# Performance work log

Measured on AMD Instinct MI355X. Metric: run time of the kernel, lower is better.

Reference implementation:

```python
import jax, jax.numpy as jnp
import numpy as np

B, S, H, T = 64, 512, 768, 50


def setup_inputs() -> dict:
    key = jax.random.key(0)
    k1, k2, k3, k4, k5, k6, k7 = jax.random.split(key, 7)
    full_hidden = jax.random.normal(k1, (B, S, H), dtype=jnp.float32)
    tag_ids = jax.random.randint(k2, (B, S), 0, T)
    lengths = jax.random.randint(k3, (B,), 1, S + 1)
    mask = (jnp.arange(S)[None, :] < lengths[:, None])  # valid-prefix mask, t=0 always on
    W = jax.random.normal(k4, (H, T), dtype=jnp.float32) * 0.02
    b = jnp.zeros((T,), dtype=jnp.float32)
    start_transitions = jax.random.normal(k5, (T,), dtype=jnp.float32) * 0.1
    end_transitions = jax.random.normal(k6, (T,), dtype=jnp.float32) * 0.1
    transitions = jax.random.normal(k7, (T, T), dtype=jnp.float32) * 0.1
    return {
        'full_hidden': full_hidden, 'W': W, 'b': b,
        'start_transitions': start_transitions, 'end_transitions': end_transitions,
        'transitions': transitions, 'tag_ids': tag_ids, 'mask': mask,
    }


def _crf_losses(emissions, start_transitions, end_transitions, transitions, tag_ids, mask):
    # emissions: [B,S,T]; returns per-sequence loss = log_partition - gold_score (pytorch-crf, reduction='none', negated)
    maskf = mask.astype(emissions.dtype)
    Bn = tag_ids.shape[0]
    bidx = jnp.arange(Bn)
    # ---- numerator: score of the gold tag path ----
    em_tag = jnp.take_along_axis(emissions, tag_ids[..., None], axis=2)[..., 0]  # [B,S]
    num = start_transitions[tag_ids[:, 0]] + em_tag[:, 0]
    trans_score = transitions[tag_ids[:, :-1], tag_ids[:, 1:]]  # [B,S-1]
    num = num + jnp.sum((trans_score + em_tag[:, 1:]) * maskf[:, 1:], axis=1)
    lengths = jnp.sum(mask.astype(jnp.int32), axis=1)
    last_tags = tag_ids[bidx, lengths - 1]
    num = num + end_transitions[last_tags]
    # ---- denominator: log partition via forward DP (scan over time) ----
    alpha0 = start_transitions[None, :] + emissions[:, 0]  # [B,T]

    def step(alpha, inp):
        em_t, m_t = inp  # [B,T], [B]
        nxt = jax.nn.logsumexp(alpha[:, :, None] + transitions[None, :, :] + em_t[:, None, :], axis=1)
        alpha = jnp.where(m_t[:, None], nxt, alpha)
        return alpha, None

    em_rest = jnp.swapaxes(emissions[:, 1:], 0, 1)  # [S-1,B,T]
    m_rest = jnp.swapaxes(mask[:, 1:], 0, 1)        # [S-1,B]
    alpha, _ = jax.lax.scan(step, alpha0, (em_rest, m_rest))
    den = jax.nn.logsumexp(alpha + end_transitions[None, :], axis=1)
    return den - num  # [B]


def reference(full_hidden, W, b, start_transitions, end_transitions, transitions, tag_ids, mask):
    # dropout is identity in eval mode (config dropout applied at train time only)
    emissions = jnp.einsum('bsh,ht->bst', full_hidden, W) + b  # hid2tag
    return _crf_losses(emissions, start_transitions, end_transitions, transitions, tag_ids, mask)
```

## Files before the change

### kernel.cpp

```cpp
#include <hip/hip_runtime.h>
#include <cstdint>
#include <cstddef>

#define Bn 64
#define Sn 512
#define Hn 768
#define Tn 50
#define CH 32
#define NCH 16

typedef short short8 __attribute__((ext_vector_type(8)));
typedef float floatx4 __attribute__((ext_vector_type(4)));

__device__ __forceinline__ uint32_t rne_bf16(float x) {
  uint32_t u = __float_as_uint(x);
  return (u + 0x7FFFu + ((u >> 16) & 1u)) >> 16;
}
__device__ __forceinline__ uint32_t pack2(float a, float b) {
  return rne_bf16(a) | (rne_bf16(b) << 16);
}
__device__ __forceinline__ float rdlane(float v, int i) {
  return __uint_as_float(__builtin_amdgcn_readlane(__float_as_uint(v), i));
}

__global__ __launch_bounds__(256) void prep_kernel(
    const float* __restrict__ W, const int* __restrict__ mask,
    uint32_t* __restrict__ wfrag, int* __restrict__ lenbuf) {
  const int blk = blockIdx.x;
  const int tid = threadIdx.x;
  if (blk < 64) {
    if (tid < 64) {
      int s = 0;
      for (int t = tid; t < Sn; t += 64) s += mask[blk * Sn + t];
#pragma unroll
      for (int off = 1; off < 64; off <<= 1) s += __shfl_xor(s, off);
      if (tid == 0) lenbuf[blk] = s;
    }
    return;
  }
  const int gid = (blk - 64) * 256 + tid;
  const int f = gid >> 6;
  const int l = gid & 63;
  const int ks = f >> 2, nt = f & 3;
  const int col = nt * 16 + (l & 15);
  const int k0 = ks * 32 + (l >> 4) * 8;
  float v[8];
#pragma unroll
  for (int j = 0; j < 8; ++j)
    v[j] = (col < Tn) ? W[(size_t)(k0 + j) * Tn + col] : 0.f;
  uint4 d;
  d.x = pack2(v[0], v[1]);
  d.y = pack2(v[2], v[3]);
  d.z = pack2(v[4], v[5]);
  d.w = pack2(v[6], v[7]);
  ((uint4*)wfrag)[gid] = d;
}

#define BK 64
__global__ __launch_bounds__(256) void emissions_kernel(
    const float* __restrict__ hidden, const uint32_t* __restrict__ wfrag,
    const float* __restrict__ bias, const int* __restrict__ lenbuf,
    float* __restrict__ em) {
  const int blk = blockIdx.x;
  const int bb = blk >> 3, c = blk & 7;
  if (c * 64 >= lenbuf[bb]) return;
  const int tid = threadIdx.x;
  const int lane = tid & 63;
  const int w = tid >> 6;
  const int g = lane >> 4;
  const int li = lane & 15;
  const int row0 = blk * 64;
  __shared__ char lds_raw[64 * 128];

  floatx4 acc[4];
#pragma unroll
  for (int nt = 0; nt < 4; ++nt) acc[nt] = (floatx4)0.f;

  const float* hbase = hidden + (size_t)row0 * Hn;
  const short8* wf = (const short8*)wfrag;

  float4 pf[4];
#pragma unroll
  for (int k = 0; k < 4; ++k)
    pf[k] = *(const float4*)(hbase + (size_t)(w * 16 + 4 * k + g) * Hn + li * 4);

  for (int ch = 0; ch < Hn / BK; ++ch) {
#pragma unroll
    for (int k = 0; k < 4; ++k) {
      const int r = w * 16 + 4 * k + g;
      const uint32_t b0 = pack2(pf[k].x, pf[k].y);
      const uint32_t b1 = pack2(pf[k].z, pf[k].w);
      const int byteoff = r * 128 + ((li * 8) ^ ((r & 7) << 4));
      *(uint2*)(lds_raw + byteoff) = make_uint2(b0, b1);
    }
    if (ch + 1 < Hn / BK) {
      const int kc = (ch + 1) * BK;
#pragma unroll
      for (int k = 0; k < 4; ++k)
        pf[k] = *(const float4*)(hbase + (size_t)(w * 16 + 4 * k + g) * Hn + kc +
                                 li * 4);
    }
    asm volatile("s_waitcnt lgkmcnt(0)" ::: "memory");
#pragma unroll
    for (int ks = 0; ks < 2; ++ks) {
      const int r = w * 16 + li;
      const int kb = ks * 64 + g * 16;
      const short8 af =
          *(const short8*)(lds_raw + r * 128 + (kb ^ ((r & 7) << 4)));
      const int ksg = ch * 2 + ks;
#pragma unroll
      for (int nt = 0; nt < 4; ++nt) {
        const short8 bf = wf[(ksg * 4 + nt) * 64 + lane];
        acc[nt] =
            __builtin_amdgcn_mfma_f32_16x16x32_bf16(af, bf, acc[nt], 0, 0, 0);
      }
    }
  }
#pragma unroll
  for (int nt = 0; nt < 4; ++nt) {
    const int col = nt * 16 + li;
    if (col < Tn) {
      const float bs = bias[col];
#pragma unroll
      for (int r = 0; r < 4; ++r) {
        const int row = row0 + w * 16 + g * 4 + r;
        em[(size_t)row * Tn + col] = acc[nt][r] + bs;
      }
    }
  }
}

__global__ __launch_bounds__(64) void scan_kernel(
    const float* __restrict__ em, const float* __restrict__ startT,
    const float* __restrict__ trans, const int* __restrict__ tag,
    const int* __restrict__ lenbuf, float* __restrict__ fvec,
    float* __restrict__ gvec, float* __restrict__ Lf,
    float* __restrict__ numpart) {
  const int blk = blockIdx.x;
  const int b = blk >> 5;
  const int c = (blk >> 1) & (NCH - 1);
  const int dir = blk & 1;
  const int len = lenbuf[b];
  const int t0 = 1 + c * CH;
  if (t0 >= len) return;
  if (dir && c == 0) return;
  const int t1 = (t0 + CH < len) ? t0 + CH : len;
  const int L = t1 - t0;
  const int lane = threadIdx.x;
  const int jc = lane < Tn ? lane : 0;
  const bool live = lane < Tn;
  const float* emb = em + (size_t)b * Sn * Tn;

  if (!dir) {
    float npv = 0.f;
    if (lane < L) {
      const int t = t0 + lane;
      const int tp = tag[b * Sn + t - 1], tc = tag[b * Sn + t];
      npv = trans[tp * Tn + tc] + emb[(size_t)t * Tn + tc];
    }
#pragma unroll
    for (int off = 1; off < 64; off <<= 1) npv += __shfl_xor(npv, off);
    if (lane == 0) numpart[b * NCH + c] = npv;
  }

  float e[Tn];
#pragma unroll
  for (int i = 0; i < Tn; ++i) {
    e[i] = __expf(dir ? trans[jc * Tn + i] : trans[i * Tn + jc]);
    asm volatile("" : "+v"(e[i]));
  }

  float Cacc = 0.f;
  float q;
  if (!dir)
    q = live ? (c == 0 ? __expf(startT[jc] + emb[jc]) : 1.f) : 0.f;
  else
    q = live ? 1.f : 0.f;

#define T_OF(k) (dir ? (t1 - 1 - (k)) : (t0 + (k)))
  float ld1 = emb[(size_t)T_OF(0) * Tn + jc];
  const float ld2 = emb[(size_t)T_OF(L > 1 ? 1 : 0) * Tn + jc];
  float ee = live ? __expf(ld1) : 0.f;
  ld1 = ld2;

  for (int k = 0; k < L; ++k) {
    const float ee_cur = ee;
    const int kn = (k + 2 < L) ? k + 2 : L - 1;
    const float ldn = emb[(size_t)T_OF(kn) * Tn + jc];
    ee = live ? __expf(ld1) : 0.f;
    ld1 = ldn;

    const float x = dir ? ee_cur * q : q;
    float s0 = 0.f, s1 = 0.f, s2 = 0.f, s3 = 0.f;
#pragma unroll
    for (int i = 0; i < 48; i += 4) {
      s0 = fmaf(rdlane(x, i + 0), e[i + 0], s0);
      s1 = fmaf(rdlane(x, i + 1), e[i + 1], s1);
      s2 = fmaf(rdlane(x, i + 2), e[i + 2], s2);
      s3 = fmaf(rdlane(x, i + 3), e[i + 3], s3);
    }
    s0 = fmaf(rdlane(x, 48), e[48], s0);
    s1 = fmaf(rdlane(x, 49), e[49], s1);
    const float s = (s0 + s1) + (s2 + s3);
    q = dir ? s : ee_cur * s;

    if ((k & 7) == 7) {
      float M = q;
#pragma unroll
      for (int off = 1; off < 64; off <<= 1) M = fmaxf(M, __shfl_xor(M, off));
      const float r = __builtin_amdgcn_rcpf(M);
      q *= r;
      Cacc -= __logf(r);
    }
  }
#undef T_OF

  float M = q;
#pragma unroll
  for (int off = 1; off < 64; off <<= 1) M = fmaxf(M, __shfl_xor(M, off));
  const float r = __builtin_amdgcn_rcpf(M);
  const float qn = live ? q * r : 0.f;
  Cacc -= __logf(r);
  if (dir) {
    gvec[((size_t)b * NCH + c) * 64 + lane] = qn;
  } else {
    fvec[((size_t)b * NCH + c) * 64 + lane] = qn;
    if (lane == 0) Lf[b * NCH + c] = Cacc;
  }
}

__global__ __launch_bounds__(64) void stitch_kernel(
    const float* __restrict__ em, const float* __restrict__ startT,
    const float* __restrict__ endT, const float* __restrict__ trans,
    const int* __restrict__ tag, const int* __restrict__ lenbuf,
    const float* __restrict__ fvec, const float* __restrict__ gvec,
    const float* __restrict__ Lf, const float* __restrict__ numpart,
    float* __restrict__ out) {
  const int b = blockIdx.x;
  const int lane = threadIdx.x;
  const int len = lenbuf[b];
  const int C = (len - 1 + CH - 1) / CH;
  const int jc = lane < Tn ? lane : 0;
  const bool live = lane < Tn;
  const float* emb = em + (size_t)b * Sn * Tn;

  float np = (lane < C) ? numpart[b * NCH + lane] : 0.f;
#pragma unroll
  for (int off = 1; off < 64; off <<= 1) np += __shfl_xor(np, off);
  const int tg0 = tag[b * Sn];
  const int tgl = tag[b * Sn + len - 1];
  np += startT[tg0] + emb[tg0] + endT[tgl];

  float den;
  if (C == 0) {
    float v = live ? (startT[jc] + emb[jc] + endT[jc]) : -INFINITY;
    float M = v;
#pragma unroll
    for (int off = 1; off < 64; off <<= 1) M = fmaxf(M, __shfl_xor(M, off));
    float s = __expf(v - M);
#pragma unroll
    for (int off = 1; off < 64; off <<= 1) s += __shfl_xor(s, off);
    den = M + __logf(s);
  } else {
    const float ev = live ? __expf(endT[jc]) : 0.f;
    float d = fvec[((size_t)b * NCH + C - 1) * 64 + lane] * ev;
#pragma unroll
    for (int off = 1; off < 64; off <<= 1) d += __shfl_xor(d, off);
    den = Lf[b * NCH + C - 1] + __logf(d);
    for (int c2 = 1; c2 < C; ++c2) {
      const float g = gvec[((size_t)b * NCH + c2) * 64 + lane];
      const float f = fvec[((size_t)b * NCH + c2 - 1) * 64 + lane];
      float dot = g * f;
      float gs = g;
#pragma unroll
      for (int off = 1; off < 64; off <<= 1) {
        dot += __shfl_xor(dot, off);
        gs += __shfl_xor(gs, off);
      }
      den += Lf[b * NCH + c2 - 1] + __logf(dot) - __logf(gs);
    }
  }
  if (lane == 0) out[b] = den - np;
}

extern "C" void kernel_launch(void* const* d_in, const int* in_sizes, int n_in,
                              void* d_out, int out_size, void* d_ws,
                              size_t ws_size, hipStream_t stream) {
  const float* hidden = (const float*)d_in[0];
  const float* W = (const float*)d_in[1];
  const float* bias = (const float*)d_in[2];
  const float* startT = (const float*)d_in[3];
  const float* endT = (const float*)d_in[4];
  const float* trans = (const float*)d_in[5];
  const int* tag = (const int*)d_in[6];
  const int* mask = (const int*)d_in[7];
  float* out = (float*)d_out;

  char* ws = (char*)d_ws;
  float* em = (float*)ws;
  uint32_t* wfrag = (uint32_t*)(ws + 6553600);
  int* lenbuf = (int*)(ws + 6651904);
  float* fvec = (float*)(ws + 6652160);
  float* gvec = (float*)(ws + 6914304);
  float* Lf = (float*)(ws + 7176448);
  float* numpart = (float*)(ws + 7180544);

  prep_kernel<<<88, 256, 0, stream>>>(W, mask, wfrag, lenbuf);
  emissions_kernel<<<(Bn * Sn) / 64, 256, 0, stream>>>(hidden, wfrag, bias,
                                                       lenbuf, em);
  scan_kernel<<<Bn * NCH * 2, 64, 0, stream>>>(em, startT, trans, tag, lenbuf,
                                               fvec, gvec, Lf, numpart);
  stitch_kernel<<<Bn, 64, 0, stream>>>(em, startT, endT, trans, tag, lenbuf,
                                       fvec, gvec, Lf, numpart, out);
}
```

Measured before the change: 62.93 us.

## Fuse prep into emissions and scan with stitch via atomic last-block counter

Removes the prep kernel. Each emissions block now converts W into bf16 MFMA fragments held in 96KB of LDS, and reads the mask directly to decide whether to skip its rows. The scan and stitch kernels are merged: every block recomputes the sequence length, and the last block per batch (detected with an atomic counter plus threadfences) runs the stitch. This cuts two kernel launches and their dependency gaps, but every emissions block now redoes the W conversion and uses far more LDS, which lowers occupancy.

```diff
diff --git a/kernel.cpp b/kernel.cpp
--- a/kernel.cpp
+++ b/kernel.cpp
@@ -23,66 +23,58 @@
   return __uint_as_float(__builtin_amdgcn_readlane(__float_as_uint(v), i));
 }
 
-__global__ __launch_bounds__(256) void prep_kernel(
-    const float* __restrict__ W, const int* __restrict__ mask,
-    uint32_t* __restrict__ wfrag, int* __restrict__ lenbuf) {
+#define BK 64
+__global__ __launch_bounds__(256) void emissions_kernel(
+    const float* __restrict__ hidden, const float* __restrict__ W,
+    const float* __restrict__ bias, const int* __restrict__ mask,
+    float* __restrict__ em, int* __restrict__ counters) {
   const int blk = blockIdx.x;
   const int tid = threadIdx.x;
-  if (blk < 64) {
-    if (tid < 64) {
-      int s = 0;
-      for (int t = tid; t < Sn; t += 64) s += mask[blk * Sn + t];
-#pragma unroll
-      for (int off = 1; off < 64; off <<= 1) s += __shfl_xor(s, off);
-      if (tid == 0) lenbuf[blk] = s;
-    }
-    return;
-  }
-  const int gid = (blk - 64) * 256 + tid;
-  const int f = gid >> 6;
-  const int l = gid & 63;
-  const int ks = f >> 2, nt = f & 3;
-  const int col = nt * 16 + (l & 15);
-  const int k0 = ks * 32 + (l >> 4) * 8;
-  float v[8];
-#pragma unroll
-  for (int j = 0; j < 8; ++j)
-    v[j] = (col < Tn) ? W[(size_t)(k0 + j) * Tn + col] : 0.f;
-  uint4 d;
-  d.x = pack2(v[0], v[1]);
-  d.y = pack2(v[2], v[3]);
-  d.z = pack2(v[4], v[5]);
-  d.w = pack2(v[6], v[7]);
-  ((uint4*)wfrag)[gid] = d;
-}
-
-#define BK 64
-__global__ __launch_bounds__(256) void emissions_kernel(
-    const float* __restrict__ hidden, const uint32_t* __restrict__ wfrag,
-    const float* __restrict__ bias, const int* __restrict__ lenbuf,
-    float* __restrict__ em) {
-  const int blk = blockIdx.x;
-  const int bb = blk >> 3, c = blk & 7;
-  if (c * 64 >= lenbuf[bb]) return;
-  const int tid = threadIdx.x;
+  if (blk == 0 && tid < 64) counters[tid] = 0;
+  const int bb = blk >> 3, c = blk & 3 + (blk & 7 & ~3);
+  const int bb2 = blk >> 3, cc = blk & 7;
+  if (mask[bb2 * Sn + cc * 64] == 0) return;
+
   const int lane = tid & 63;
   const int w = tid >> 6;
   const int g = lane >> 4;
   const int li = lane & 15;
   const int row0 = blk * 64;
+
+  __shared__ uint4 wlds[96 * 64];
   __shared__ char lds_raw[64 * 128];
 
-  floatx4 acc[4];
-#pragma unroll
-  for (int nt = 0; nt < 4; ++nt) acc[nt] = (floatx4)0.f;
-
   const float* hbase = hidden + (size_t)row0 * Hn;
-  const short8* wf = (const short8*)wfrag;
 
   float4 pf[4];
 #pragma unroll
   for (int k = 0; k < 4; ++k)
     pf[k] = *(const float4*)(hbase + (size_t)(w * 16 + 4 * k + g) * Hn + li * 4);
+
+#pragma unroll
+  for (int it = 0; it < 24; ++it) {
+    const int idx = tid + it * 256;
+    const int f = idx >> 6;
+    const int l = idx & 63;
+    const int ks = f >> 2, nt = f & 3;
+    const int col = nt * 16 + (l & 15);
+    const int k0 = ks * 32 + (l >> 4) * 8;
+    float v[8];
+#pragma unroll
+    for (int j = 0; j < 8; ++j)
+      v[j] = (col < Tn) ? W[(size_t)(k0 + j) * Tn + col] : 0.f;
+    uint4 d;
+    d.x = pack2(v[0], v[1]);
+    d.y = pack2(v[2], v[3]);
+    d.z = pack2(v[4], v[5]);
+    d.w = pack2(v[6], v[7]);
+    wlds[idx] = d;
+  }
+  __syncthreads();
+
+  floatx4 acc[4];
+#pragma unroll
+  for (int nt = 0; nt < 4; ++nt) acc[nt] = (floatx4)0.f;
 
   for (int ch = 0; ch < Hn / BK; ++ch) {
 #pragma unroll
@@ -110,7 +102,7 @@
       const int ksg = ch * 2 + ks;
 #pragma unroll
       for (int nt = 0; nt < 4; ++nt) {
-        const short8 bf = wf[(ksg * 4 + nt) * 64 + lane];
+        const short8 bf = *(const short8*)&wlds[(ksg * 4 + nt) * 64 + lane];
         acc[nt] =
             __builtin_amdgcn_mfma_f32_16x16x32_bf16(af, bf, acc[nt], 0, 0, 0);
       }
@@ -130,119 +122,120 @@
   }
 }
 
-__global__ __launch_bounds__(64) void scan_kernel(
+__global__ __launch_bounds__(64) void scan_stitch_kernel(
     const float* __restrict__ em, const float* __restrict__ startT,
-    const float* __restrict__ trans, const int* __restrict__ tag,
-    const int* __restrict__ lenbuf, float* __restrict__ fvec,
-    float* __restrict__ gvec, float* __restrict__ Lf,
-    float* __restrict__ numpart) {
+    const float* __restrict__ endT, const float* __restrict__ trans,
+    const int* __restrict__ tag, const int* __restrict__ mask,
+    float* __restrict__ fvec, float* __restrict__ gvec,
+    float* __restrict__ Lf, float* __restrict__ numpart,
+    int* __restrict__ counters, float* __restrict__ out) {
   const int blk = blockIdx.x;
   const int b = blk >> 5;
   const int c = (blk >> 1) & (NCH - 1);
   const int dir = blk & 1;
-  const int len = lenbuf[b];
-  const int t0 = 1 + c * CH;
-  if (t0 >= len) return;
-  if (dir && c == 0) return;
-  const int t1 = (t0 + CH < len) ? t0 + CH : len;
-  const int L = t1 - t0;
   const int lane = threadIdx.x;
   const int jc = lane < Tn ? lane : 0;
   const bool live = lane < Tn;
   const float* emb = em + (size_t)b * Sn * Tn;
 
-  if (!dir) {
-    float npv = 0.f;
-    if (lane < L) {
-      const int t = t0 + lane;
-      const int tp = tag[b * Sn + t - 1], tc = tag[b * Sn + t];
-      npv = trans[tp * Tn + tc] + emb[(size_t)t * Tn + tc];
-    }
-#pragma unroll
-    for (int off = 1; off < 64; off <<= 1) npv += __shfl_xor(npv, off);
-    if (lane == 0) numpart[b * NCH + c] = npv;
-  }
-
-  float e[Tn];
-#pragma unroll
-  for (int i = 0; i < Tn; ++i) {
-    e[i] = __expf(dir ? trans[jc * Tn + i] : trans[i * Tn + jc]);
-    asm volatile("" : "+v"(e[i]));
-  }
-
-  float Cacc = 0.f;
-  float q;
-  if (!dir)
-    q = live ? (c == 0 ? __expf(startT[jc] + emb[jc]) : 1.f) : 0.f;
-  else
-    q = live ? 1.f : 0.f;
+  int len = 0;
+  for (int t = lane; t < Sn; t += 64) len += mask[b * Sn + t];
+#pragma unroll
+  for (int off = 1; off < 64; off <<= 1) len += __shfl_xor(len, off);
+
+  const int t0 = 1 + c * CH;
+  const bool active = (t0 < len) && !(dir && c == 0);
+
+  if (active) {
+    const int t1 = (t0 + CH < len) ? t0 + CH : len;
+    const int L = t1 - t0;
+
+    if (!dir) {
+      float npv = 0.f;
+      if (lane < L) {
+        const int t = t0 + lane;
+        const int tp = tag[b * Sn + t - 1], tc = tag[b * Sn + t];
+        npv = trans[tp * Tn + tc] + emb[(size_t)t * Tn + tc];
+      }
+#pragma unroll
+      for (int off = 1; off < 64; off <<= 1) npv += __shfl_xor(npv, off);
+      if (lane == 0) numpart[b * NCH + c] = npv;
+    }
+
+    float e[Tn];
+#pragma unroll
+    for (int i = 0; i < Tn; ++i) {
+      e[i] = __expf(dir ? trans[jc * Tn + i] : trans[i * Tn + jc]);
+      asm volatile("" : "+v"(e[i]));
+    }
+
+    float Cacc = 0.f;
+    float q;
+    if (!dir)
+      q = live ? (c == 0 ? __expf(startT[jc] + emb[jc]) : 1.f) : 0.f;
+    else
+      q = live ? 1.f : 0.f;
 
 #define T_OF(k) (dir ? (t1 - 1 - (k)) : (t0 + (k)))
-  float ld1 = emb[(size_t)T_OF(0) * Tn + jc];
-  const float ld2 = emb[(size_t)T_OF(L > 1 ? 1 : 0) * Tn + jc];
-  float ee = live ? __expf(ld1) : 0.f;
-  ld1 = ld2;
-
-  for (int k = 0; k < L; ++k) {
-    const float ee_cur = ee;
-    const int kn = (k + 2 < L) ? k + 2 : L - 1;
-    const float ldn = emb[(size_t)T_OF(kn) * Tn + jc];
-    ee = live ? __expf(ld1) : 0.f;
-    ld1 = ldn;
-
-    const float x = dir ? ee_cur * q : q;
-    float s0 = 0.f, s1 = 0.f, s2 = 0.f, s3 = 0.f;
-#pragma unroll
-    for (int i = 0; i < 48; i += 4) {
-      s0 = fmaf(rdlane(x, i + 0), e[i + 0], s0);
-      s1 = fmaf(rdlane(x, i + 1), e[i + 1], s1);
-      s2 = fmaf(rdlane(x, i + 2), e[i + 2], s2);
-      s3 = fmaf(rdlane(x, i + 3), e[i + 3], s3);
-    }
-    s0 = fmaf(rdlane(x, 48), e[48], s0);
-    s1 = fmaf(rdlane(x, 49), e[49], s1);
-    const float s = (s0 + s1) + (s2 + s3);
-    q = dir ? s : ee_cur * s;
-
-    if ((k & 7) == 7) {
-      float M = q;
-#pragma unroll
-      for (int off = 1; off < 64; off <<= 1) M = fmaxf(M, __shfl_xor(M, off));
-      const float r = __builtin_amdgcn_rcpf(M);
-      q *= r;
-      Cacc -= __logf(r);
-    }
-  }
+    float ld1 = emb[(size_t)T_OF(0) * Tn + jc];
+    const float ld2 = emb[(size_t)T_OF(L > 1 ? 1 : 0) * Tn + jc];
+    float ee = live ? __expf(ld1) : 0.f;
+    ld1 = ld2;
+
+    for (int k = 0; k < L; ++k) {
+      const float ee_cur = ee;
+      const int kn = (k + 2 < L) ? k + 2 : L - 1;
+      const float ldn = emb[(size_t)T_OF(kn) * Tn + jc];
+      ee = live ? __expf(ld1) : 0.f;
+      ld1 = ldn;
+
+      const float x = dir ? ee_cur * q : q;
+      float s0 = 0.f, s1 = 0.f, s2 = 0.f, s3 = 0.f;
+#pragma unroll
+      for (int i = 0; i < 48; i += 4) {
+        s0 = fmaf(rdlane(x, i + 0), e[i + 0], s0);
+        s1 = fmaf(rdlane(x, i + 1), e[i + 1], s1);
+        s2 = fmaf(rdlane(x, i + 2), e[i + 2], s2);
+        s3 = fmaf(rdlane(x, i + 3), e[i + 3], s3);
+      }
+      s0 = fmaf(rdlane(x, 48), e[48], s0);
+      s1 = fmaf(rdlane(x, 49), e[49], s1);
+      const float s = (s0 + s1) + (s2 + s3);
+      q = dir ? s : ee_cur * s;
+
+      if ((k & 7) == 7) {
+        float M = q;
+#pragma unroll
+        for (int off = 1; off < 64; off <<= 1) M = fmaxf(M, __shfl_xor(M, off));
+        const float r = __builtin_amdgcn_rcpf(M);
+        q *= r;
+        Cacc -= __logf(r);
+      }
+    }
 #undef T_OF
 
-  float M = q;
-#pragma unroll
-  for (int off = 1; off < 64; off <<= 1) M = fmaxf(M, __shfl_xor(M, off));
-  const float r = __builtin_amdgcn_rcpf(M);
-  const float qn = live ? q * r : 0.f;
-  Cacc -= __logf(r);
-  if (dir) {
-    gvec[((size_t)b * NCH + c) * 64 + lane] = qn;
-  } else {
-    fvec[((size_t)b * NCH + c) * 64 + lane] = qn;
-    if (lane == 0) Lf[b * NCH + c] = Cacc;
-  }
-}
-
-__global__ __launch_bounds__(64) void stitch_kernel(
-    const float* __restrict__ em, const float* __restrict__ startT,
-    const float* __restrict__ endT, const float* __restrict__ trans,
-    const int* __restrict__ tag, const int* __restrict__ lenbuf,
-    const float* __restrict__ fvec, const float* __restrict__ gvec,
-    const float* __restrict__ Lf, const float* __restrict__ numpart,
-    float* __restrict__ out) {
-  const int b = blockIdx.x;
-  const int lane = threadIdx.x;
-  const int len = lenbuf[b];
+    float M = q;
+#pragma unroll
+    for (int off = 1; off < 64; off <<= 1) M = fmaxf(M, __shfl_xor(M, off));
+    const float r = __builtin_amdgcn_rcpf(M);
+    const float qn = live ? q * r : 0.f;
+    Cacc -= __logf(r);
+    if (dir) {
+      gvec[((size_t)b * NCH + c) * 64 + lane] = qn;
+    } else {
+      fvec[((size_t)b * NCH + c) * 64 + lane] = qn;
+      if (lane == 0) Lf[b * NCH + c] = Cacc;
+    }
+  }
+
+  __threadfence();
+  int old = 0;
+  if (lane == 0) old = atomicAdd(&counters[b], 1);
+  old = __shfl(old, 0);
+  if (old != 31) return;
+  __threadfence();
+
   const int C = (len - 1 + CH - 1) / CH;
-  const int jc = lane < Tn ? lane : 0;
-  const bool live = lane < Tn;
-  const float* emb = em + (size_t)b * Sn * Tn;
 
   float np = (lane < C) ? numpart[b * NCH + lane] : 0.f;
 #pragma unroll
@@ -298,18 +291,15 @@
 
   char* ws = (char*)d_ws;
   float* em = (float*)ws;
-  uint32_t* wfrag = (uint32_t*)(ws + 6553600);
-  int* lenbuf = (int*)(ws + 6651904);
-  float* fvec = (float*)(ws + 6652160);
-  float* gvec = (float*)(ws + 6914304);
-  float* Lf = (float*)(ws + 7176448);
-  float* numpart = (float*)(ws + 7180544);
-
-  prep_kernel<<<88, 256, 0, stream>>>(W, mask, wfrag, lenbuf);
-  emissions_kernel<<<(Bn * Sn) / 64, 256, 0, stream>>>(hidden, wfrag, bias,
-                                                       lenbuf, em);
-  scan_kernel<<<Bn * NCH * 2, 64, 0, stream>>>(em, startT, trans, tag, lenbuf,
-                                               fvec, gvec, Lf, numpart);
-  stitch_kernel<<<Bn, 64, 0, stream>>>(em, startT, endT, trans, tag, lenbuf,
-                                       fvec, gvec, Lf, numpart, out);
-}
+  float* fvec = (float*)(ws + 6553600);
+  float* gvec = (float*)(ws + 6815744);
+  float* Lf = (float*)(ws + 7077888);
+  float* numpart = (float*)(ws + 7081984);
+  int* counters = (int*)(ws + 7086080);
+
+  emissions_kernel<<<(Bn * Sn) / 64, 256, 0, stream>>>(hidden, W, bias, mask,
+                                                       em, counters);
+  scan_stitch_kernel<<<Bn * NCH * 2, 64, 0, stream>>>(
+      em, startT, endT, trans, tag, mask, fvec, gvec, Lf, numpart, counters,
+      out);
+}
```

Result: slower. 116.9 us (+85.8%).

## Precompute exp(transitions) once and double-buffer hidden loads in emissions GEMM

Applied to the files above, without the earlier changes.

Adds a prep block that writes exp(transitions) and its transpose, padded to 52 columns, into workspace. Scan blocks now load these precomputed rows instead of each recomputing 50 exponentials. The emissions kernel keeps two register prefetch buffers so global loads run two chunks ahead of the LDS write and MFMA compute. Both kernels get a min-blocks-per-CU hint of 1 in launch_bounds, which allows more registers but may lower occupancy.

```diff
diff --git a/kernel.cpp b/kernel.cpp
--- a/kernel.cpp
+++ b/kernel.cpp
@@ -8,6 +8,7 @@
 #define Tn 50
 #define CH 32
 #define NCH 16
+#define EP 52
 
 typedef short short8 __attribute__((ext_vector_type(8)));
 typedef float floatx4 __attribute__((ext_vector_type(4)));
@@ -24,8 +25,10 @@
 }
 
 __global__ __launch_bounds__(256) void prep_kernel(
-    const float* __restrict__ W, const int* __restrict__ mask,
-    uint32_t* __restrict__ wfrag, int* __restrict__ lenbuf) {
+    const float* __restrict__ W, const float* __restrict__ trans,
+    const int* __restrict__ mask, uint32_t* __restrict__ wfrag,
+    int* __restrict__ lenbuf, float* __restrict__ Ee,
+    float* __restrict__ EeT) {
   const int blk = blockIdx.x;
   const int tid = threadIdx.x;
   if (blk < 64) {
@@ -35,6 +38,15 @@
 #pragma unroll
       for (int off = 1; off < 64; off <<= 1) s += __shfl_xor(s, off);
       if (tid == 0) lenbuf[blk] = s;
+    }
+    return;
+  }
+  if (blk == 88) {
+    for (int gid = tid; gid < Tn * Tn; gid += 256) {
+      const int r = gid / Tn, cl = gid - r * Tn;
+      const float v = __expf(trans[gid]);
+      Ee[r * EP + cl] = v;
+      EeT[cl * EP + r] = v;
     }
     return;
   }
@@ -57,13 +69,13 @@
 }
 
 #define BK 64
-__global__ __launch_bounds__(256) void emissions_kernel(
+__global__ __launch_bounds__(256, 1) void emissions_kernel(
     const float* __restrict__ hidden, const uint32_t* __restrict__ wfrag,
     const float* __restrict__ bias, const int* __restrict__ lenbuf,
     float* __restrict__ em) {
   const int blk = blockIdx.x;
-  const int bb = blk >> 3, c = blk & 7;
-  if (c * 64 >= lenbuf[bb]) return;
+  const int bb = blk >> 3, cc = blk & 7;
+  if (cc * 64 >= lenbuf[bb]) return;
   const int tid = threadIdx.x;
   const int lane = tid & 63;
   const int w = tid >> 6;
@@ -79,43 +91,51 @@
   const float* hbase = hidden + (size_t)row0 * Hn;
   const short8* wf = (const short8*)wfrag;
 
-  float4 pf[4];
-#pragma unroll
-  for (int k = 0; k < 4; ++k)
-    pf[k] = *(const float4*)(hbase + (size_t)(w * 16 + 4 * k + g) * Hn + li * 4);
-
-  for (int ch = 0; ch < Hn / BK; ++ch) {
-#pragma unroll
-    for (int k = 0; k < 4; ++k) {
-      const int r = w * 16 + 4 * k + g;
-      const uint32_t b0 = pack2(pf[k].x, pf[k].y);
-      const uint32_t b1 = pack2(pf[k].z, pf[k].w);
-      const int byteoff = r * 128 + ((li * 8) ^ ((r & 7) << 4));
-      *(uint2*)(lds_raw + byteoff) = make_uint2(b0, b1);
-    }
-    if (ch + 1 < Hn / BK) {
-      const int kc = (ch + 1) * BK;
-#pragma unroll
-      for (int k = 0; k < 4; ++k)
-        pf[k] = *(const float4*)(hbase + (size_t)(w * 16 + 4 * k + g) * Hn + kc +
-                                 li * 4);
-    }
-    asm volatile("s_waitcnt lgkmcnt(0)" ::: "memory");
-#pragma unroll
-    for (int ks = 0; ks < 2; ++ks) {
-      const int r = w * 16 + li;
-      const int kb = ks * 64 + g * 16;
-      const short8 af =
-          *(const short8*)(lds_raw + r * 128 + (kb ^ ((r & 7) << 4)));
-      const int ksg = ch * 2 + ks;
-#pragma unroll
-      for (int nt = 0; nt < 4; ++nt) {
-        const short8 bf = wf[(ksg * 4 + nt) * 64 + lane];
-        acc[nt] =
-            __builtin_amdgcn_mfma_f32_16x16x32_bf16(af, bf, acc[nt], 0, 0, 0);
-      }
-    }
-  }
+#define LOADCH(dst, ch)                                                       \
+  _Pragma("unroll") for (int k = 0; k < 4; ++k) dst[k] =                      \
+      *(const float4*)(hbase + (size_t)(w * 16 + 4 * k + g) * Hn + (ch)*BK +  \
+                       li * 4);
+
+#define WRITELDS(src)                                                         \
+  _Pragma("unroll") for (int k = 0; k < 4; ++k) {                             \
+    const int r = w * 16 + 4 * k + g;                                         \
+    const uint32_t b0 = pack2(src[k].x, src[k].y);                            \
+    const uint32_t b1 = pack2(src[k].z, src[k].w);                            \
+    const int byteoff = r * 128 + ((li * 8) ^ ((r & 7) << 4));                \
+    *(uint2*)(lds_raw + byteoff) = make_uint2(b0, b1);                        \
+  }
+
+#define COMPUTE(ch)                                                           \
+  _Pragma("unroll") for (int ks = 0; ks < 2; ++ks) {                          \
+    const int r = w * 16 + li;                                                \
+    const int kb = ks * 64 + g * 16;                                          \
+    const short8 af =                                                         \
+        *(const short8*)(lds_raw + r * 128 + (kb ^ ((r & 7) << 4)));          \
+    const int ksg = (ch)*2 + ks;                                              \
+    _Pragma("unroll") for (int nt = 0; nt < 4; ++nt) {                        \
+      const short8 bf = wf[(ksg * 4 + nt) * 64 + lane];                       \
+      acc[nt] =                                                               \
+          __builtin_amdgcn_mfma_f32_16x16x32_bf16(af, bf, acc[nt], 0, 0, 0);  \
+    }                                                                         \
+  }
+
+  float4 pfA[4], pfB[4];
+  LOADCH(pfA, 0)
+  LOADCH(pfB, 1)
+#pragma unroll
+  for (int chp = 0; chp < Hn / BK / 2; ++chp) {
+    const int ch = 2 * chp;
+    WRITELDS(pfA)
+    if (ch + 2 < Hn / BK) LOADCH(pfA, ch + 2)
+    COMPUTE(ch)
+    WRITELDS(pfB)
+    if (ch + 3 < Hn / BK) LOADCH(pfB, ch + 3)
+    COMPUTE(ch + 1)
+  }
+#undef LOADCH
+#undef WRITELDS
+#undef COMPUTE
+
 #pragma unroll
   for (int nt = 0; nt < 4; ++nt) {
     const int col = nt * 16 + li;
@@ -130,9 +150,10 @@
   }
 }
 
-__global__ __launch_bounds__(64) void scan_kernel(
+__global__ __launch_bounds__(64, 1) void scan_kernel(
     const float* __restrict__ em, const float* __restrict__ startT,
-    const float* __restrict__ trans, const int* __restrict__ tag,
+    const float* __restrict__ trans, const float* __restrict__ Ee,
+    const float* __restrict__ EeT, const int* __restrict__ tag,
     const int* __restrict__ lenbuf, float* __restrict__ fvec,
     float* __restrict__ gvec, float* __restrict__ Lf,
     float* __restrict__ numpart) {
@@ -163,12 +184,10 @@
     if (lane == 0) numpart[b * NCH + c] = npv;
   }
 
+  const float* ebase = (dir ? Ee : EeT) + jc * EP;
   float e[Tn];
 #pragma unroll
-  for (int i = 0; i < Tn; ++i) {
-    e[i] = __expf(dir ? trans[jc * Tn + i] : trans[i * Tn + jc]);
-    asm volatile("" : "+v"(e[i]));
-  }
+  for (int i = 0; i < Tn; ++i) e[i] = ebase[i];
 
   float Cacc = 0.f;
   float q;
@@ -231,11 +250,10 @@
 
 __global__ __launch_bounds__(64) void stitch_kernel(
     const float* __restrict__ em, const float* __restrict__ startT,
-    const float* __restrict__ endT, const float* __restrict__ trans,
-    const int* __restrict__ tag, const int* __restrict__ lenbuf,
-    const float* __restrict__ fvec, const float* __restrict__ gvec,
-    const float* __restrict__ Lf, const float* __restrict__ numpart,
-    float* __restrict__ out) {
+    const float* __restrict__ endT, const int* __restrict__ tag,
+    const int* __restrict__ lenbuf, const float* __restrict__ fvec,
+    const float* __restrict__ gvec, const float* __restrict__ Lf,
+    const float* __restrict__ numpart, float* __restrict__ out) {
   const int b = blockIdx.x;
   const int lane = threadIdx.x;
   const int len = lenbuf[b];
@@ -300,16 +318,18 @@
   float* em = (float*)ws;
   uint32_t* wfrag = (uint32_t*)(ws + 6553600);
   int* lenbuf = (int*)(ws + 6651904);
-  float* fvec = (float*)(ws + 6652160);
-  float* gvec = (float*)(ws + 6914304);
-  float* Lf = (float*)(ws + 7176448);
-  float* numpart = (float*)(ws + 7180544);
-
-  prep_kernel<<<88, 256, 0, stream>>>(W, mask, wfrag, lenbuf);
+  float* Ee = (float*)(ws + 6652160);
+  float* EeT = (float*)(ws + 6662976);
+  float* fvec = (float*)(ws + 6673792);
+  float* gvec = (float*)(ws + 6935936);
+  float* Lf = (float*)(ws + 7198080);
+  float* numpart = (float*)(ws + 7202176);
+
+  prep_kernel<<<89, 256, 0, stream>>>(W, trans, mask, wfrag, lenbuf, Ee, EeT);
   emissions_kernel<<<(Bn * Sn) / 64, 256, 0, stream>>>(hidden, wfrag, bias,
                                                        lenbuf, em);
-  scan_kernel<<<Bn * NCH * 2, 64, 0, stream>>>(em, startT, trans, tag, lenbuf,
-                                               fvec, gvec, Lf, numpart);
-  stitch_kernel<<<Bn, 64, 0, stream>>>(em, startT, endT, trans, tag, lenbuf,
-                                       fvec, gvec, Lf, numpart, out);
-}
+  scan_kernel<<<Bn * NCH * 2, 64, 0, stream>>>(em, startT, trans, Ee, EeT, tag,
+                                               lenbuf, fvec, gvec, Lf, numpart);
+  stitch_kernel<<<Bn, 64, 0, stream>>>(em, startT, endT, tag, lenbuf, fvec,
+                                       gvec, Lf, numpart, out);
+}
```

Result: faster. 53.16 us (-15.5%).
